# Optimization experiments

Hardware: AMD Instinct MI355X
Metric: run time of the kernel (lower is better)

Reference implementation:

```python
import jax, jax.numpy as jnp
import numpy as np

H = 16
D_MODEL = 1024
D_K = D_MODEL // H
MAX_REL = 16
REL_VOCAB = 2 * MAX_REL + 1


def _rel_pos_ids(seq_len):
    r = jnp.arange(seq_len)
    dist = r[None, :] - r[:, None]                      # [S,S]
    return jnp.clip(dist, -MAX_REL, MAX_REL) + MAX_REL  # in [0, 2*MAX_REL]


def setup_inputs() -> dict:
    key = jax.random.key(0)
    ks = jax.random.split(key, 16)
    B, S = 2, 2048
    f32 = jnp.float32
    inp = {
        "query": jax.random.normal(ks[0], (B, S, D_MODEL), f32),
        "key": jax.random.normal(ks[1], (B, S, D_MODEL), f32),
        "value": jax.random.normal(ks[2], (B, S, D_MODEL), f32),
        # four nn.Linear(d_model, d_model): W [out,in], b [out]
        "Wq": jax.random.normal(ks[3], (D_MODEL, D_MODEL), f32) * 0.02,
        "bq": jnp.zeros((D_MODEL,), f32),
        "Wk": jax.random.normal(ks[4], (D_MODEL, D_MODEL), f32) * 0.02,
        "bk": jnp.zeros((D_MODEL,), f32),
        "Wv": jax.random.normal(ks[5], (D_MODEL, D_MODEL), f32) * 0.02,
        "bv": jnp.zeros((D_MODEL,), f32),
        "Wo": jax.random.normal(ks[6], (D_MODEL, D_MODEL), f32) * 0.02,
        "bo": jnp.zeros((D_MODEL,), f32),
        # relative-position embedding tables (keys and values)
        "rel_k_table": jax.random.normal(ks[7], (REL_VOCAB, D_K), f32) * 0.02,
        "rel_v_table": jax.random.normal(ks[8], (REL_VOCAB, D_K), f32) * 0.02,
    }
    return inp


def reference(query, key, value, Wq, bq, Wk, bk, Wv, bv, Wo, bo,
              rel_k_table, rel_v_table):
    B, S, E = query.shape
    ids = _rel_pos_ids(S)                    # [S,S] int
    rel_k = rel_k_table[ids]                 # [S,S,d_k]
    rel_v = rel_v_table[ids]                 # [S,S,d_k]

    def proj(x, W, b):
        y = x @ W.T + b                      # [B,S,E]
        return y.reshape(B, S, H, D_K).transpose(0, 2, 1, 3)  # [B,H,S,d_k]

    q = proj(query, Wq, bq)
    k = proj(key, Wk, bk)
    v = proj(value, Wv, bv)

    # NOTE: original has no 1/sqrt(d_k) scaling and ignores mask — faithful.
    logits = jnp.einsum('bhqd,bhkd->bhqk', q, k) \
           + jnp.einsum('bhqd,qkd->bhqk', q, rel_k)
    w = jax.nn.softmax(logits, axis=-1)      # [B,H,S,S]

    x = jnp.einsum('bhqk,bhkd->bhqd', w, v) \
      + jnp.einsum('bhqk,qkd->bhqd', w, rel_v)

    x = x.transpose(0, 2, 1, 3).reshape(B, S, H * D_K)
    return x @ Wo.T + bo
```

## Files before the change

kernel.cpp:

```cpp
#include <hip/hip_runtime.h>
#include <hip/hip_bf16.h>

typedef unsigned short u16;
typedef __attribute__((ext_vector_type(8))) short short8;
typedef __attribute__((ext_vector_type(4))) short short4_t;
typedef __attribute__((ext_vector_type(4))) float f32x4;

#define MFMA16(a, b, c) __builtin_amdgcn_mfma_f32_16x16x32_bf16((a), (b), (c), 0, 0, 0)

#if __has_builtin(__builtin_amdgcn_mfma_f32_16x16x16bf16_1k)
#define MFMAK16(a, b, c) __builtin_amdgcn_mfma_f32_16x16x16bf16_1k((a), (b), (c), 0, 0, 0)
#elif __has_builtin(__builtin_amdgcn_mfma_f32_16x16x16_bf16)
#define MFMAK16(a, b, c) __builtin_amdgcn_mfma_f32_16x16x16_bf16((a), (b), (c), 0, 0, 0)
#else
__device__ __forceinline__ f32x4 mfmak16_asm(short4_t a, short4_t b, f32x4 c) {
  asm("v_mfma_f32_16x16x16_bf16 %0, %1, %2, %0" : "+v"(c) : "v"(a), "v"(b));
  return c;
}
#define MFMAK16(a, b, c) mfmak16_asm((a), (b), (c))
#endif

#define GLOAD_LDS16(gp, lp)                                          \
  __builtin_amdgcn_global_load_lds(                                  \
      (const __attribute__((address_space(1))) void*)(gp),           \
      (__attribute__((address_space(3))) void*)(lp), 16, 0, 0)
#define SBAR() asm volatile("s_barrier" ::: "memory")
#define WAIT_LGKM0() asm volatile("s_waitcnt lgkmcnt(0)" ::: "memory")

__device__ __forceinline__ float us2f(u16 u) {
  union { unsigned int i; float f; } c; c.i = ((unsigned int)u) << 16; return c.f;
}
__device__ __forceinline__ u16 f2us(float f) {
  union { float f; unsigned int i; } c; c.f = f;
  return (u16)((c.i + 0x7fffu + ((c.i >> 16) & 1u)) >> 16);
}
__device__ __forceinline__ unsigned int f2us2(float a, float b) {
  union { __hip_bfloat162 h; unsigned int u; } c;
  c.h = __float22bfloat162_rn(float2{a, b});
  return c.u;
}

__global__ __launch_bounds__(256) void cvt_all_kernel(
    const float* x0, const float* x1, const float* x2, const float* w0,
    const float* w1, const float* w2, const float* w3, u16* y0, u16* y1,
    u16* y2, u16* z0, u16* z1, u16* z2, u16* z3) {
  const int z = blockIdx.z;
  const float* src; u16* dst; int n;
  switch (z) {
    case 0: src = x0; dst = y0; n = 4194304; break;
    case 1: src = x1; dst = y1; n = 4194304; break;
    case 2: src = x2; dst = y2; n = 4194304; break;
    case 3: src = w0; dst = z0; n = 1048576; break;
    case 4: src = w1; dst = z1; n = 1048576; break;
    case 5: src = w2; dst = z2; n = 1048576; break;
    default: src = w3; dst = z3; n = 1048576; break;
  }
  const int i = (blockIdx.x * 256 + threadIdx.x) * 8;
  if (i < n) {
    const float4 a = *(const float4*)(src + i);
    const float4 b = *(const float4*)(src + i + 4);
    unsigned int o[4];
    o[0] = f2us2(a.x, a.y); o[1] = f2us2(a.z, a.w);
    o[2] = f2us2(b.x, b.y); o[3] = f2us2(b.z, b.w);
    *(uint4*)(dst + i) = *(uint4*)o;
  }
}

__global__ __launch_bounds__(256) void cvt_relk_kernel(const float* relk, u16* relkb) {
  const int i = blockIdx.x * 256 + threadIdx.x;
  if (i < 4096) relkb[i] = (i < 2112) ? f2us(relk[i]) : (u16)0;
}

template <bool SCATTER, typename OUT>
__device__ __forceinline__ void gemm_body(const u16* __restrict__ X,
                                          const u16* __restrict__ W,
                                          const float* __restrict__ bias,
                                          OUT* __restrict__ Y, int row0, int col0,
                                          bool vt) {
  __shared__ __align__(16) u16 As[128 * 64];
  __shared__ __align__(16) u16 Bs[128 * 64];
  const int tid = threadIdx.x;
  const int lane = tid & 63;
  const int wid = tid >> 6;
  const int wm = wid >> 1, wn = wid & 1;
  const int l15 = lane & 15, l16 = lane >> 4;
  const int lrow = lane >> 3;
  const int lchunk = (lane & 7) ^ lrow;

  f32x4 acc[4][4];
#pragma unroll
  for (int i = 0; i < 4; i++)
#pragma unroll
    for (int j = 0; j < 4; j++) acc[i][j] = (f32x4){0.f, 0.f, 0.f, 0.f};

  for (int k0 = 0; k0 < 1024; k0 += 64) {
#pragma unroll
    for (int i = 0; i < 4; i++) {
      const int rb = wid * 32 + i * 8;
      GLOAD_LDS16(X + (size_t)(row0 + rb + lrow) * 1024 + k0 + lchunk * 8, &As[rb * 64]);
      GLOAD_LDS16(W + (size_t)(col0 + rb + lrow) * 1024 + k0 + lchunk * 8, &Bs[rb * 64]);
    }
    __syncthreads();
#pragma unroll
    for (int kk = 0; kk < 2; kk++) {
      const int ch = kk * 4 + l16;
      short8 af[4], bfr[4];
#pragma unroll
      for (int t = 0; t < 4; t++) {
        const int m = wm * 64 + t * 16 + l15;
        af[t] = *(const short8*)&As[m * 64 + ((ch ^ (m & 7)) * 8)];
        const int n = wn * 64 + t * 16 + l15;
        bfr[t] = *(const short8*)&Bs[n * 64 + ((ch ^ (n & 7)) * 8)];
      }
#pragma unroll
      for (int tm = 0; tm < 4; tm++)
#pragma unroll
        for (int tn = 0; tn < 4; tn++)
          acc[tm][tn] = MFMA16(af[tm], bfr[tn], acc[tm][tn]);
    }
    __syncthreads();
  }

#pragma unroll
  for (int tn = 0; tn < 4; tn++) {
    const int col = col0 + wn * 64 + tn * 16 + l15;
    const float bv = bias[col];
#pragma unroll
    for (int tm = 0; tm < 4; tm++) {
      const int rowb = row0 + wm * 64 + tm * 16 + l16 * 4;
      if (SCATTER) {
        const int bb = rowb >> 11, ss = rowb & 2047;
        const int hh = col >> 6, dd = col & 63;
        if (vt) {
          unsigned int o[2];
          o[0] = f2us2(acc[tm][tn][0] + bv, acc[tm][tn][1] + bv);
          o[1] = f2us2(acc[tm][tn][2] + bv, acc[tm][tn][3] + bv);
          *(short4_t*)&((u16*)Y)[(((size_t)(bb * 16 + hh)) * 64 + dd) * 2048 + ss] =
              *(short4_t*)o;
        } else {
#pragma unroll
          for (int r = 0; r < 4; r++)
            ((u16*)Y)[(((size_t)(bb * 16 + hh)) * 2048 + ss + r) * 64 + dd] =
                f2us(acc[tm][tn][r] + bv);
        }
      } else {
#pragma unroll
        for (int r = 0; r < 4; r++)
          Y[(size_t)(rowb + r) * 1024 + col] = (OUT)(acc[tm][tn][r] + bv);
      }
    }
  }
}

__global__ __launch_bounds__(256) void qkv_kernel(
    const u16* Xq, const u16* Xk, const u16* Xv, const u16* Wq, const u16* Wk,
    const u16* Wv, const float* bq, const float* bk, const float* bv, u16* Yq,
    u16* Yk, u16* Yv) {
  const int z = blockIdx.z;
  const u16* X = z == 0 ? Xq : (z == 1 ? Xk : Xv);
  const u16* W = z == 0 ? Wq : (z == 1 ? Wk : Wv);
  const float* bi = z == 0 ? bq : (z == 1 ? bk : bv);
  u16* Y = z == 0 ? Yq : (z == 1 ? Yk : Yv);
  gemm_body<true, u16>(X, W, bi, Y, blockIdx.x * 128, blockIdx.y * 128, z == 2);
}

__global__ __launch_bounds__(256) void oproj_kernel(const u16* Xc, const u16* Wo,
                                                    const float* bo, float* out) {
  gemm_body<false, float>(Xc, Wo, bo, out, blockIdx.x * 128, blockIdx.y * 128, false);
}

__global__ __launch_bounds__(256) void attn_kernel(
    const u16* __restrict__ Qg, const u16* __restrict__ Kg,
    const u16* __restrict__ Vtg, const u16* __restrict__ relkb,
    const float* __restrict__ relv, u16* __restrict__ ctx) {
  __shared__ __align__(16) u16 KVs[2][8192];
  __shared__ __align__(4) u16 qrelJ[64 * 33];
  __shared__ __align__(4) u16 wsum[64 * 31];

  const int tid = threadIdx.x, lane = tid & 63, wid = tid >> 6;
  const int l15 = lane & 15, l16 = lane >> 4;
  const int bh = blockIdx.x;
  const int b = bh >> 4, h = bh & 15;
  const int q0 = blockIdx.y * 64;
  const u16* Qb = Qg + (size_t)bh * 2048 * 64;
  const u16* Kb = Kg + (size_t)bh * 2048 * 64;
  const u16* Vtb = Vtg + (size_t)bh * 64 * 2048;

  const int lrow = lane >> 3;
  const int lchunk = (lane & 7) ^ lrow;
  const int qw = wid * 16;
  const int kq4 = l16 * 4;
  const int qrow = qw + l15;

  u16* Qs = &KVs[1][0];

#pragma unroll
  for (int i = 0; i < 2; i++) {
    const int rb = wid * 16 + i * 8;
    GLOAD_LDS16(Qb + (size_t)(q0 + rb + lrow) * 64 + lchunk * 8, &Qs[rb * 64]);
  }
  for (int idx = tid; idx < 64 * 31 / 2; idx += 256) ((unsigned int*)wsum)[idx] = 0u;
  __syncthreads();

  short8 aq[2];
  {
    const int m = qw + l15;
    aq[0] = *(const short8*)&Qs[m * 64 + ((l16 ^ (m & 7)) * 8)];
    aq[1] = *(const short8*)&Qs[m * 64 + (((4 + l16) ^ (m & 7)) * 8)];
  }

#pragma unroll
  for (int i = 0; i < 2; i++) {
    const int rb = wid * 16 + i * 8;
    GLOAD_LDS16(Kb + (size_t)(rb + lrow) * 64 + lchunk * 8, &KVs[0][rb * 64]);
  }
#pragma unroll
  for (int i = 0; i < 2; i++) {
    const int rb = wid * 16 + i * 8;
    GLOAD_LDS16(Vtb + (size_t)(rb + lrow) * 2048 + lchunk * 8, &KVs[0][4096 + rb * 64]);
  }

  {
    f32x4 qa[3];
#pragma unroll
    for (int nt = 0; nt < 3; nt++) {
      qa[nt] = (f32x4){0.f, 0.f, 0.f, 0.f};
#pragma unroll
      for (int kk = 0; kk < 2; kk++) {
        const short8 bf =
            *(const short8*)(relkb + (nt * 16 + l15) * 64 + kk * 32 + l16 * 8);
        qa[nt] = MFMA16(aq[kk], bf, qa[nt]);
      }
    }
#pragma unroll
    for (int nt = 0; nt < 3; nt++) {
      if (nt < 2 || l15 == 0) {
#pragma unroll
        for (int r = 0; r < 4; r++)
          qrelJ[(qw + kq4 + r) * 33 + nt * 16 + l15] = f2us(qa[nt][r]);
      }
    }
  }
  WAIT_LGKM0();
  const float q0r = us2f(qrelJ[qrow * 33 + 0]);
  const float q32r = us2f(qrelJ[qrow * 33 + 32]);

  float l_acc = 0.f, wl_acc = 0.f, wr_acc = 0.f;
  f32x4 Oacc[4];
#pragma unroll
  for (int t = 0; t < 4; t++) Oacc[t] = (f32x4){0.f, 0.f, 0.f, 0.f};

  for (int kt = 0; kt < 32; kt++) {
    SBAR();
    u16* KVc = &KVs[kt & 1][0];
    u16* KVn = &KVs[(kt & 1) ^ 1][0];
    if (kt < 31) {
      const int kn = (kt + 1) * 64;
#pragma unroll
      for (int i = 0; i < 2; i++) {
        const int rb = wid * 16 + i * 8;
        GLOAD_LDS16(Kb + (size_t)(kn + rb + lrow) * 64 + lchunk * 8, &KVn[rb * 64]);
      }
#pragma unroll
      for (int i = 0; i < 2; i++) {
        const int rb = wid * 16 + i * 8;
        GLOAD_LDS16(Vtb + (size_t)(rb + lrow) * 2048 + kn + lchunk * 8,
                    &KVn[4096 + rb * 64]);
      }
      asm volatile("s_waitcnt vmcnt(4)" ::: "memory");
    } else {
      asm volatile("s_waitcnt vmcnt(0)" ::: "memory");
    }
    SBAR();

    const int k0 = kt * 64;

    f32x4 sac[4];
#pragma unroll
    for (int t = 0; t < 4; t++) sac[t] = (f32x4){0.f, 0.f, 0.f, 0.f};
#pragma unroll
    for (int kk = 0; kk < 2; kk++) {
      const int ch = kk * 4 + l16;
#pragma unroll
      for (int tn = 0; tn < 4; tn++) {
        const int n = tn * 16 + l15;
        const short8 bk = *(const short8*)&KVc[n * 64 + ((ch ^ (n & 7)) * 8)];
        sac[tn] = MFMA16(bk, aq[kk], sac[tn]);
      }
    }

    float p[4][4];
    if (k0 + 79 <= q0 || k0 >= q0 + 79) {
      const float eb = (k0 < q0) ? q0r : q32r;
      float ts = 0.f;
#pragma unroll
      for (int tn = 0; tn < 4; tn++)
#pragma unroll
        for (int r = 0; r < 4; r++) {
          p[tn][r] = __expf(sac[tn][r] + eb);
          ts += p[tn][r];
        }
      l_acc += ts;
      if (k0 < q0) wl_acc += ts; else wr_acc += ts;
    } else {
#pragma unroll
      for (int tn = 0; tn < 4; tn++) {
#pragma unroll
        for (int r = 0; r < 4; r++) {
          const int kg = k0 + tn * 16 + kq4 + r;
          const int dlt = kg - (q0 + qrow);
          const int jj = (dlt < -16 ? -16 : (dlt > 16 ? 16 : dlt)) + 16;
          const float pv = __expf(sac[tn][r] + us2f(qrelJ[qrow * 33 + jj]));
          p[tn][r] = pv;
          l_acc += pv;
          if (dlt <= -16) wl_acc += pv;
          else if (dlt >= 16) wr_acc += pv;
          else wsum[qrow * 31 + (dlt + 15)] = f2us(pv);
        }
      }
    }

    short4_t pf[4];
#pragma unroll
    for (int tn = 0; tn < 4; tn++) {
      union { unsigned int u[2]; short4_t s; } c;
      c.u[0] = f2us2(p[tn][0], p[tn][1]);
      c.u[1] = f2us2(p[tn][2], p[tn][3]);
      pf[tn] = c.s;
    }

#pragma unroll
    for (int td = 0; td < 4; td++) {
      const int row = td * 16 + l15;
      const int rs = row & 7;
#pragma unroll
      for (int kk = 0; kk < 4; kk++) {
        const short4_t vf = *(const short4_t*)&KVc[4096 + row * 64 +
                                                   (((kk * 2 + (l16 >> 1)) ^ rs) * 8) +
                                                   (l16 & 1) * 4];
        Oacc[td] = MFMAK16(vf, pf[kk], Oacc[td]);
      }
    }
  }

  l_acc += __shfl_xor(l_acc, 16); l_acc += __shfl_xor(l_acc, 32);
  wl_acc += __shfl_xor(wl_acc, 16); wl_acc += __shfl_xor(wl_acc, 32);
  wr_acc += __shfl_xor(wr_acc, 16); wr_acc += __shfl_xor(wr_acc, 32);
  const float linv = 1.f / l_acc;
  wl_acc *= linv; wr_acc *= linv;

#pragma unroll
  for (int td = 0; td < 4; td++) {
    const f32x4 rv0 = *(const f32x4*)&relv[td * 16 + kq4];
    const f32x4 rv32 = *(const f32x4*)&relv[32 * 64 + td * 16 + kq4];
#pragma unroll
    for (int r = 0; r < 4; r++)
      Oacc[td][r] = Oacc[td][r] * linv + wl_acc * rv0[r] + wr_acc * rv32[r];
  }
  for (int j = 1; j <= 31; j++) {
    const float wv = us2f(wsum[qrow * 31 + (j - 1)]) * linv;
#pragma unroll
    for (int td = 0; td < 4; td++) {
      const f32x4 rv = *(const f32x4*)&relv[j * 64 + td * 16 + kq4];
#pragma unroll
      for (int r = 0; r < 4; r++) Oacc[td][r] += wv * rv[r];
    }
  }
  const size_t srow = ((size_t)b * 2048 + q0 + qrow) * 1024 + h * 64;
#pragma unroll
  for (int td = 0; td < 4; td++)
#pragma unroll
    for (int r = 0; r < 4; r++)
      ctx[srow + td * 16 + kq4 + r] = f2us(Oacc[td][r]);
}

extern "C" void kernel_launch(void* const* d_in, const int* in_sizes, int n_in,
                              void* d_out, int out_size, void* d_ws, size_t ws_size,
                              hipStream_t stream) {
  u16* qb = (u16*)d_ws;
  u16* kb = qb + 4194304;
  u16* vtb = kb + 4194304;
  u16* ctx = vtb + 4194304;
  u16* Xq = ctx + 4194304;
  u16* Xk = Xq + 4194304;
  u16* Xv = Xk + 4194304;
  u16* Wqb = Xv + 4194304;
  u16* Wkb = Wqb + 1048576;
  u16* Wvb = Wkb + 1048576;
  u16* Wob = Wvb + 1048576;
  u16* relkb = Wob + 1048576;

  const float* bq = (const float*)d_in[4];
  const float* bk = (const float*)d_in[6];
  const float* bv = (const float*)d_in[8];
  const float* bo = (const float*)d_in[10];
  const float* relk = (const float*)d_in[11];
  const float* relv = (const float*)d_in[12];

  dim3 blk(256);
  cvt_all_kernel<<<dim3(2048, 1, 7), blk, 0, stream>>>(
      (const float*)d_in[0], (const float*)d_in[1], (const float*)d_in[2],
      (const float*)d_in[3], (const float*)d_in[5], (const float*)d_in[7],
      (const float*)d_in[9], Xq, Xk, Xv, Wqb, Wkb, Wvb, Wob);
  cvt_relk_kernel<<<16, blk, 0, stream>>>(relk, relkb);
  qkv_kernel<<<dim3(32, 8, 3), blk, 0, stream>>>(Xq, Xk, Xv, Wqb, Wkb, Wvb, bq,
                                                 bk, bv, qb, kb, vtb);
  attn_kernel<<<dim3(32, 32), blk, 0, stream>>>(qb, kb, vtb, relkb, relv, ctx);
  oproj_kernel<<<dim3(32, 8), blk, 0, stream>>>(ctx, Wob, bo, (float*)d_out);
}
```

Baseline: 281.3 us.

## Single-buffer attention K/V for occupancy, stage GEMM and attention outputs through LDS

The attention kernel drops double-buffered K/V prefetch in favour of one LDS buffer with a synchronous load each tile, and requests 6 blocks per CU through launch bounds. This cuts LDS and register use to raise occupancy, at the cost of exposed load latency per tile. The QK^T compute is fused per column tile with the exp and bf16 packing, which shortens score lifetimes. The QKV projection epilogue and the attention context write now go through an LDS transpose so global stores become vectorised and coalesced instead of scattered 2-byte stores.

```diff
diff --git a/kernel.cpp b/kernel.cpp
--- a/kernel.cpp
+++ b/kernel.cpp
@@ -26,6 +26,7 @@
       (__attribute__((address_space(3))) void*)(lp), 16, 0, 0)
 #define SBAR() asm volatile("s_barrier" ::: "memory")
 #define WAIT_LGKM0() asm volatile("s_waitcnt lgkmcnt(0)" ::: "memory")
+#define WAIT_VM0() asm volatile("s_waitcnt vmcnt(0)" ::: "memory")
 
 __device__ __forceinline__ float us2f(u16 u) {
   union { unsigned int i; float f; } c; c.i = ((unsigned int)u) << 16; return c.f;
@@ -71,14 +72,14 @@
   if (i < 4096) relkb[i] = (i < 2112) ? f2us(relk[i]) : (u16)0;
 }
 
-template <bool SCATTER, typename OUT>
-__device__ __forceinline__ void gemm_body(const u16* __restrict__ X,
+template <int MODE, typename OUT>
+__device__ __forceinline__ void gemm_body(u16* __restrict__ SM,
+                                          const u16* __restrict__ X,
                                           const u16* __restrict__ W,
                                           const float* __restrict__ bias,
-                                          OUT* __restrict__ Y, int row0, int col0,
-                                          bool vt) {
-  __shared__ __align__(16) u16 As[128 * 64];
-  __shared__ __align__(16) u16 Bs[128 * 64];
+                                          OUT* __restrict__ Y, int row0, int col0) {
+  u16* As = SM;
+  u16* Bs = SM + 8192;
   const int tid = threadIdx.x;
   const int lane = tid & 63;
   const int wid = tid >> 6;
@@ -121,32 +122,69 @@
     __syncthreads();
   }
 
-#pragma unroll
-  for (int tn = 0; tn < 4; tn++) {
-    const int col = col0 + wn * 64 + tn * 16 + l15;
-    const float bv = bias[col];
-#pragma unroll
-    for (int tm = 0; tm < 4; tm++) {
-      const int rowb = row0 + wm * 64 + tm * 16 + l16 * 4;
-      if (SCATTER) {
-        const int bb = rowb >> 11, ss = rowb & 2047;
-        const int hh = col >> 6, dd = col & 63;
-        if (vt) {
-          unsigned int o[2];
-          o[0] = f2us2(acc[tm][tn][0] + bv, acc[tm][tn][1] + bv);
-          o[1] = f2us2(acc[tm][tn][2] + bv, acc[tm][tn][3] + bv);
-          *(short4_t*)&((u16*)Y)[(((size_t)(bb * 16 + hh)) * 64 + dd) * 2048 + ss] =
-              *(short4_t*)o;
-        } else {
-#pragma unroll
-          for (int r = 0; r < 4; r++)
-            ((u16*)Y)[(((size_t)(bb * 16 + hh)) * 2048 + ss + r) * 64 + dd] =
-                f2us(acc[tm][tn][r] + bv);
-        }
-      } else {
+  if (MODE == 0) {
+#pragma unroll
+    for (int tn = 0; tn < 4; tn++) {
+      const int col = col0 + wn * 64 + tn * 16 + l15;
+      const float bv = bias[col];
+#pragma unroll
+      for (int tm = 0; tm < 4; tm++) {
+        const int rowb = row0 + wm * 64 + tm * 16 + l16 * 4;
 #pragma unroll
         for (int r = 0; r < 4; r++)
           Y[(size_t)(rowb + r) * 1024 + col] = (OUT)(acc[tm][tn][r] + bv);
+      }
+    }
+  } else {
+    u16* T = SM;
+    const int bb = row0 >> 11;
+    const int sbase = row0 & 2047;
+#pragma unroll
+    for (int pass = 0; pass < 2; pass++) {
+      __syncthreads();
+      if (wm == pass) {
+#pragma unroll
+        for (int tn = 0; tn < 4; tn++) {
+          const int coll = wn * 64 + tn * 16 + l15;
+          const float bv = bias[col0 + coll];
+#pragma unroll
+          for (int tm = 0; tm < 4; tm++) {
+            if (MODE == 1) {
+#pragma unroll
+              for (int r = 0; r < 4; r++)
+                T[(tm * 16 + l16 * 4 + r) * 136 + coll] = f2us(acc[tm][tn][r] + bv);
+            } else {
+              unsigned int o[2];
+              o[0] = f2us2(acc[tm][tn][0] + bv, acc[tm][tn][1] + bv);
+              o[1] = f2us2(acc[tm][tn][2] + bv, acc[tm][tn][3] + bv);
+              *(short4_t*)&T[coll * 72 + tm * 16 + l16 * 4] = *(short4_t*)o;
+            }
+          }
+        }
+      }
+      __syncthreads();
+      if (MODE == 1) {
+#pragma unroll
+        for (int i = 0; i < 8; i++) {
+          const int idx = tid + i * 256;
+          const int srow = idx >> 5, c4 = idx & 31;
+          const short4_t v = *(const short4_t*)&T[srow * 136 + c4 * 4];
+          const int col = col0 + c4 * 4;
+          const int hh = col >> 6, dd = col & 63;
+          const int s = sbase + pass * 64 + srow;
+          *(short4_t*)&((u16*)Y)[(((size_t)(bb * 16 + hh)) * 2048 + s) * 64 + dd] = v;
+        }
+      } else {
+#pragma unroll
+        for (int i = 0; i < 4; i++) {
+          const int idx = tid + i * 256;
+          const int cl = idx >> 3, sc = idx & 7;
+          const short8 v = *(const short8*)&T[cl * 72 + sc * 8];
+          const int col = col0 + cl;
+          const int hh = col >> 6, dd = col & 63;
+          const int s = sbase + pass * 64 + sc * 8;
+          *(short8*)&((u16*)Y)[(((size_t)(bb * 16 + hh)) * 64 + dd) * 2048 + s] = v;
+        }
       }
     }
   }
@@ -156,26 +194,31 @@
     const u16* Xq, const u16* Xk, const u16* Xv, const u16* Wq, const u16* Wk,
     const u16* Wv, const float* bq, const float* bk, const float* bv, u16* Yq,
     u16* Yk, u16* Yv) {
+  __shared__ __align__(16) u16 SM[16384];
   const int z = blockIdx.z;
   const u16* X = z == 0 ? Xq : (z == 1 ? Xk : Xv);
   const u16* W = z == 0 ? Wq : (z == 1 ? Wk : Wv);
   const float* bi = z == 0 ? bq : (z == 1 ? bk : bv);
   u16* Y = z == 0 ? Yq : (z == 1 ? Yk : Yv);
-  gemm_body<true, u16>(X, W, bi, Y, blockIdx.x * 128, blockIdx.y * 128, z == 2);
+  if (z == 2)
+    gemm_body<2, u16>(SM, X, W, bi, Y, blockIdx.x * 128, blockIdx.y * 128);
+  else
+    gemm_body<1, u16>(SM, X, W, bi, Y, blockIdx.x * 128, blockIdx.y * 128);
 }
 
 __global__ __launch_bounds__(256) void oproj_kernel(const u16* Xc, const u16* Wo,
                                                     const float* bo, float* out) {
-  gemm_body<false, float>(Xc, Wo, bo, out, blockIdx.x * 128, blockIdx.y * 128, false);
-}
-
-__global__ __launch_bounds__(256) void attn_kernel(
+  __shared__ __align__(16) u16 SM[16384];
+  gemm_body<0, float>(SM, Xc, Wo, bo, out, blockIdx.x * 128, blockIdx.y * 128);
+}
+
+__global__ __launch_bounds__(256, 6) void attn_kernel(
     const u16* __restrict__ Qg, const u16* __restrict__ Kg,
     const u16* __restrict__ Vtg, const u16* __restrict__ relkb,
     const float* __restrict__ relv, u16* __restrict__ ctx) {
-  __shared__ __align__(16) u16 KVs[2][8192];
-  __shared__ __align__(4) u16 qrelJ[64 * 33];
-  __shared__ __align__(4) u16 wsum[64 * 31];
+  __shared__ __align__(16) u16 KV[8192];
+  __shared__ __align__(16) u16 qrelJ[64 * 33];
+  __shared__ __align__(16) u16 wsum[64 * 31];
 
   const int tid = threadIdx.x, lane = tid & 63, wid = tid >> 6;
   const int l15 = lane & 15, l16 = lane >> 4;
@@ -192,34 +235,20 @@
   const int kq4 = l16 * 4;
   const int qrow = qw + l15;
 
-  u16* Qs = &KVs[1][0];
-
 #pragma unroll
   for (int i = 0; i < 2; i++) {
     const int rb = wid * 16 + i * 8;
-    GLOAD_LDS16(Qb + (size_t)(q0 + rb + lrow) * 64 + lchunk * 8, &Qs[rb * 64]);
-  }
-  for (int idx = tid; idx < 64 * 31 / 2; idx += 256) ((unsigned int*)wsum)[idx] = 0u;
+    GLOAD_LDS16(Qb + (size_t)(q0 + rb + lrow) * 64 + lchunk * 8, &KV[rb * 64]);
+  }
+  for (int idx = tid; idx < 992; idx += 256) ((unsigned int*)wsum)[idx] = 0u;
   __syncthreads();
 
   short8 aq[2];
   {
     const int m = qw + l15;
-    aq[0] = *(const short8*)&Qs[m * 64 + ((l16 ^ (m & 7)) * 8)];
-    aq[1] = *(const short8*)&Qs[m * 64 + (((4 + l16) ^ (m & 7)) * 8)];
-  }
-
-#pragma unroll
-  for (int i = 0; i < 2; i++) {
-    const int rb = wid * 16 + i * 8;
-    GLOAD_LDS16(Kb + (size_t)(rb + lrow) * 64 + lchunk * 8, &KVs[0][rb * 64]);
-  }
-#pragma unroll
-  for (int i = 0; i < 2; i++) {
-    const int rb = wid * 16 + i * 8;
-    GLOAD_LDS16(Vtb + (size_t)(rb + lrow) * 2048 + lchunk * 8, &KVs[0][4096 + rb * 64]);
-  }
-
+    aq[0] = *(const short8*)&KV[m * 64 + ((l16 ^ (m & 7)) * 8)];
+    aq[1] = *(const short8*)&KV[m * 64 + (((4 + l16) ^ (m & 7)) * 8)];
+  }
   {
     f32x4 qa[3];
 #pragma unroll
@@ -252,81 +281,72 @@
 
   for (int kt = 0; kt < 32; kt++) {
     SBAR();
-    u16* KVc = &KVs[kt & 1][0];
-    u16* KVn = &KVs[(kt & 1) ^ 1][0];
-    if (kt < 31) {
-      const int kn = (kt + 1) * 64;
-#pragma unroll
-      for (int i = 0; i < 2; i++) {
-        const int rb = wid * 16 + i * 8;
-        GLOAD_LDS16(Kb + (size_t)(kn + rb + lrow) * 64 + lchunk * 8, &KVn[rb * 64]);
-      }
-#pragma unroll
-      for (int i = 0; i < 2; i++) {
-        const int rb = wid * 16 + i * 8;
-        GLOAD_LDS16(Vtb + (size_t)(rb + lrow) * 2048 + kn + lchunk * 8,
-                    &KVn[4096 + rb * 64]);
-      }
-      asm volatile("s_waitcnt vmcnt(4)" ::: "memory");
-    } else {
-      asm volatile("s_waitcnt vmcnt(0)" ::: "memory");
-    }
+    const int k0 = kt * 64;
+#pragma unroll
+    for (int i = 0; i < 2; i++) {
+      const int rb = wid * 16 + i * 8;
+      GLOAD_LDS16(Kb + (size_t)(k0 + rb + lrow) * 64 + lchunk * 8, &KV[rb * 64]);
+    }
+#pragma unroll
+    for (int i = 0; i < 2; i++) {
+      const int rb = wid * 16 + i * 8;
+      GLOAD_LDS16(Vtb + (size_t)(rb + lrow) * 2048 + k0 + lchunk * 8,
+                  &KV[4096 + rb * 64]);
+    }
+    WAIT_VM0();
     SBAR();
 
-    const int k0 = kt * 64;
-
-    f32x4 sac[4];
-#pragma unroll
-    for (int t = 0; t < 4; t++) sac[t] = (f32x4){0.f, 0.f, 0.f, 0.f};
-#pragma unroll
-    for (int kk = 0; kk < 2; kk++) {
-      const int ch = kk * 4 + l16;
-#pragma unroll
-      for (int tn = 0; tn < 4; tn++) {
-        const int n = tn * 16 + l15;
-        const short8 bk = *(const short8*)&KVc[n * 64 + ((ch ^ (n & 7)) * 8)];
-        sac[tn] = MFMA16(bk, aq[kk], sac[tn]);
-      }
-    }
-
-    float p[4][4];
+    short4_t pf[4];
     if (k0 + 79 <= q0 || k0 >= q0 + 79) {
       const float eb = (k0 < q0) ? q0r : q32r;
       float ts = 0.f;
 #pragma unroll
-      for (int tn = 0; tn < 4; tn++)
-#pragma unroll
-        for (int r = 0; r < 4; r++) {
-          p[tn][r] = __expf(sac[tn][r] + eb);
-          ts += p[tn][r];
-        }
+      for (int tn = 0; tn < 4; tn++) {
+        f32x4 sac = (f32x4){0.f, 0.f, 0.f, 0.f};
+#pragma unroll
+        for (int kk = 0; kk < 2; kk++) {
+          const int n = tn * 16 + l15;
+          const short8 bk = *(const short8*)&KV[n * 64 + (((kk * 4 + l16) ^ (n & 7)) * 8)];
+          sac = MFMA16(bk, aq[kk], sac);
+        }
+        float p0 = __expf(sac[0] + eb), p1 = __expf(sac[1] + eb);
+        float p2 = __expf(sac[2] + eb), p3 = __expf(sac[3] + eb);
+        ts += (p0 + p1) + (p2 + p3);
+        union { unsigned int u[2]; short4_t s; } c;
+        c.u[0] = f2us2(p0, p1);
+        c.u[1] = f2us2(p2, p3);
+        pf[tn] = c.s;
+      }
       l_acc += ts;
       if (k0 < q0) wl_acc += ts; else wr_acc += ts;
     } else {
 #pragma unroll
       for (int tn = 0; tn < 4; tn++) {
+        f32x4 sac = (f32x4){0.f, 0.f, 0.f, 0.f};
+#pragma unroll
+        for (int kk = 0; kk < 2; kk++) {
+          const int n = tn * 16 + l15;
+          const short8 bk = *(const short8*)&KV[n * 64 + (((kk * 4 + l16) ^ (n & 7)) * 8)];
+          sac = MFMA16(bk, aq[kk], sac);
+        }
+        float pv4[4];
 #pragma unroll
         for (int r = 0; r < 4; r++) {
           const int kg = k0 + tn * 16 + kq4 + r;
           const int dlt = kg - (q0 + qrow);
           const int jj = (dlt < -16 ? -16 : (dlt > 16 ? 16 : dlt)) + 16;
-          const float pv = __expf(sac[tn][r] + us2f(qrelJ[qrow * 33 + jj]));
-          p[tn][r] = pv;
+          const float pv = __expf(sac[r] + us2f(qrelJ[qrow * 33 + jj]));
+          pv4[r] = pv;
           l_acc += pv;
           if (dlt <= -16) wl_acc += pv;
           else if (dlt >= 16) wr_acc += pv;
           else wsum[qrow * 31 + (dlt + 15)] = f2us(pv);
         }
-      }
-    }
-
-    short4_t pf[4];
-#pragma unroll
-    for (int tn = 0; tn < 4; tn++) {
-      union { unsigned int u[2]; short4_t s; } c;
-      c.u[0] = f2us2(p[tn][0], p[tn][1]);
-      c.u[1] = f2us2(p[tn][2], p[tn][3]);
-      pf[tn] = c.s;
+        union { unsigned int u[2]; short4_t s; } c;
+        c.u[0] = f2us2(pv4[0], pv4[1]);
+        c.u[1] = f2us2(pv4[2], pv4[3]);
+        pf[tn] = c.s;
+      }
     }
 
 #pragma unroll
@@ -335,9 +355,9 @@
       const int rs = row & 7;
 #pragma unroll
       for (int kk = 0; kk < 4; kk++) {
-        const short4_t vf = *(const short4_t*)&KVc[4096 + row * 64 +
-                                                   (((kk * 2 + (l16 >> 1)) ^ rs) * 8) +
-                                                   (l16 & 1) * 4];
+        const short4_t vf = *(const short4_t*)&KV[4096 + row * 64 +
+                                                  (((kk * 2 + (l16 >> 1)) ^ rs) * 8) +
+                                                  (l16 & 1) * 4];
         Oacc[td] = MFMAK16(vf, pf[kk], Oacc[td]);
       }
     }
@@ -357,6 +377,7 @@
     for (int r = 0; r < 4; r++)
       Oacc[td][r] = Oacc[td][r] * linv + wl_acc * rv0[r] + wr_acc * rv32[r];
   }
+  WAIT_LGKM0();
   for (int j = 1; j <= 31; j++) {
     const float wv = us2f(wsum[qrow * 31 + (j - 1)]) * linv;
 #pragma unroll
@@ -366,12 +387,23 @@
       for (int r = 0; r < 4; r++) Oacc[td][r] += wv * rv[r];
     }
   }
-  const size_t srow = ((size_t)b * 2048 + q0 + qrow) * 1024 + h * 64;
-#pragma unroll
-  for (int td = 0; td < 4; td++)
-#pragma unroll
-    for (int r = 0; r < 4; r++)
-      ctx[srow + td * 16 + kq4 + r] = f2us(Oacc[td][r]);
+  SBAR();
+#pragma unroll
+  for (int td = 0; td < 4; td++) {
+    unsigned int o[2];
+    o[0] = f2us2(Oacc[td][0], Oacc[td][1]);
+    o[1] = f2us2(Oacc[td][2], Oacc[td][3]);
+    *(short4_t*)&KV[qrow * 72 + td * 16 + kq4] = *(short4_t*)o;
+  }
+  WAIT_LGKM0();
+  SBAR();
+#pragma unroll
+  for (int i = 0; i < 2; i++) {
+    const int idx = tid + i * 256;
+    const int q = idx >> 3, sc = idx & 7;
+    const short8 v = *(const short8*)&KV[q * 72 + sc * 8];
+    *(short8*)&ctx[((size_t)b * 2048 + q0 + q) * 1024 + h * 64 + sc * 8] = v;
+  }
 }
 
 extern "C" void kernel_launch(void* const* d_in, const int* in_sizes, int n_in,
```

Result: faster. 269.7 us (-4.1%).
